# Kernel tuning notes

Measured on AMD Instinct MI355X. Metric: run time of the kernel, lower is better.

The kernel has to match this reference:

```python
import jax, jax.numpy as jnp
import numpy as np

IN_F = 4096
OUT_F = 4096
PACKED_IN = IN_F // 16  # 16 ternary values per int32 (2 bits each)
TOKENS = 8192


def _pack(vals_int32):
    # vals_int32: [out, packed_in, 16] with entries in {0,1,2}
    shifts = (jnp.arange(16, dtype=jnp.int32) * 2)
    return jnp.sum(vals_int32 << shifts, axis=-1).astype(jnp.int32)


def _unpack_weight(packed, scale, in_features):
    # packed: [out, packed_in] int32 -> fp32 weight [out, in_features]
    shifts = (jnp.arange(16, dtype=jnp.int32) * 2)
    vals = (packed[:, :, None] >> shifts) & 3           # [out, packed_in, 16]
    w = vals.reshape(packed.shape[0], -1)[:, :in_features]
    return (w.astype(jnp.float32) - 1.0) * scale


def setup_inputs() -> dict:
    key = jax.random.key(0)
    k1, k2 = jax.random.split(key)
    x = jax.random.normal(k1, (TOKENS, IN_F), dtype=jnp.float32)
    # mapped ternary values in {0,1,2} (i.e. w_ternary + 1), packed 2-bit
    mapped = jax.random.randint(k2, (OUT_F, PACKED_IN, 16), 0, 3, dtype=jnp.int32)
    packed_weight = _pack(mapped)
    scale = jnp.float32(0.02)
    return {"x": x, "packed_weight": packed_weight, "scale": scale}


def reference(x, packed_weight, scale):
    # dequantize ternary weight
    w = _unpack_weight(packed_weight, scale, IN_F)      # [out, in]
    # abs-max activation scaling along the last dim
    x_scale = jnp.clip(jnp.max(jnp.abs(x), axis=-1, keepdims=True), 1e-5, None)
    x_scaled = x / x_scale
    out = jnp.einsum('ti,oi->to', x_scaled, w)          # F.linear (no bias)
    return out * x_scale
```

## Files before the change

kernel.cpp:

```cpp
#include <hip/hip_runtime.h>
#include <math.h>

typedef __attribute__((ext_vector_type(4)))  int   i32x4;
typedef __attribute__((ext_vector_type(16))) int   i32x16;
typedef __attribute__((ext_vector_type(4)))  float f32x4;

namespace {
constexpr int IN_F   = 4096;
constexpr int OUT_F  = 4096;
constexpr int TOKENS = 8192;
constexpr int PACKED = IN_F / 16;

constexpr int BM   = 256;
constexpr int BN   = 128;
constexpr int BK   = 128;
constexpr int NTHR = 256;
constexpr int NT   = IN_F / BK;

constexpr size_t XQ_BYTES = (size_t)TOKENS * IN_F;
constexpr size_t XS_BYTES = (size_t)TOKENS * 4;
constexpr size_t BQ_OFF   = XQ_BYTES + XS_BYTES;
constexpr size_t BQ_BYTES = (size_t)PACKED * OUT_F * 16;
constexpr size_t WS_NEED  = BQ_OFF + BQ_BYTES;
}

__device__ __forceinline__ i32x4 unpack16(unsigned w) {
  i32x4 r;
#pragma unroll
  for (int g = 0; g < 4; ++g) {
    unsigned t = (w >> (8 * g)) & 0xFFu;
    unsigned s = (t | (t << 6) | (t << 12) | (t << 18)) & 0x03030303u;
    r[g] = (int)((((s | 0x80808080u) - 0x01010101u) ^ 0x80808080u));
  }
  return r;
}

__global__ __launch_bounds__(256)
void rowquant(const float* __restrict__ X, signed char* __restrict__ XQ,
              float* __restrict__ XS) {
  __shared__ float smax[4];
  const int row = blockIdx.x;
  const int t   = threadIdx.x;
  const float* xr = X + (size_t)row * IN_F + t * 16;

  f32x4 v[4];
  float m = 0.f;
#pragma unroll
  for (int j = 0; j < 4; ++j) {
    v[j] = *(const f32x4*)(xr + j * 4);
    m = fmaxf(m, fmaxf(fmaxf(fabsf(v[j].x), fabsf(v[j].y)),
                       fmaxf(fabsf(v[j].z), fabsf(v[j].w))));
  }
#pragma unroll
  for (int off = 32; off; off >>= 1) m = fmaxf(m, __shfl_xor(m, off, 64));
  if ((t & 63) == 0) smax[t >> 6] = m;
  __syncthreads();
  m = fmaxf(fmaxf(smax[0], smax[1]), fmaxf(smax[2], smax[3]));
  m = fmaxf(m, 1e-5f);
  const float r = 127.f / m;

  i32x4 d;
#pragma unroll
  for (int j = 0; j < 4; ++j) {
    int q0 = (int)rintf(v[j].x * r);
    int q1 = (int)rintf(v[j].y * r);
    int q2 = (int)rintf(v[j].z * r);
    int q3 = (int)rintf(v[j].w * r);
    d[j] = (q0 & 255) | ((q1 & 255) << 8) | ((q2 & 255) << 16) | ((q3 & 255) << 24);
  }
  *(i32x4*)(XQ + (size_t)row * IN_F + t * 16) = d;
  if (t == 0) XS[row] = m;
}

__global__ __launch_bounds__(256)
void unpackB(const unsigned* __restrict__ PW, signed char* __restrict__ BQ) {
  const int g = blockIdx.x * 256 + threadIdx.x;
  const int c = g >> 12;
  const int n = g & 4095;
  i32x4 u = unpack16(PW[(size_t)n * PACKED + c]);
  *(i32x4*)(BQ + ((size_t)c * OUT_F + n) * 16) = u;
}

#define STAGE_A(BUF, KT)                                                        \
  {                                                                             \
    _Pragma("unroll")                                                           \
    for (int cc = 0; cc < 2; ++cc) {                                            \
      const int c_ = w * 2 + cc;                                                \
      _Pragma("unroll")                                                         \
      for (int rb = 0; rb < 4; ++rb) {                                          \
        const signed char* src =                                                \
            XQ + (size_t)(m0 + rb * 64 + lane) * IN_F + (KT) * BK + c_ * 16;    \
        signed char* dst = lA + (BUF) * 32768 + c_ * 4096 + rb * 1024;          \
        __builtin_amdgcn_global_load_lds(                                       \
            (const __attribute__((address_space(1))) void*)src,                 \
            (__attribute__((address_space(3))) void*)dst, 16, 0, 0);            \
      }                                                                         \
    }                                                                           \
  }

#define LOAD_B(B, KT)                                                           \
  {                                                                             \
    _Pragma("unroll")                                                           \
    for (int nf = 0; nf < 2; ++nf) {                                            \
      _Pragma("unroll")                                                         \
      for (int ks = 0; ks < 4; ++ks)                                            \
        B[nf][ks] = *(const i32x4*)(BQ +                                        \
            ((size_t)((KT) * 8 + ks * 2 + h) * OUT_F + nrow[nf]) * 16);         \
      }                                                                         \
  }

#define COMPUTE_TILE(BUFOFF, B)                                                 \
  {                                                                             \
    _Pragma("unroll")                                                           \
    for (int ks = 0; ks < 4; ++ks) {                                            \
      i32x4 afr[4];                                                             \
      _Pragma("unroll")                                                         \
      for (int mf = 0; mf < 4; ++mf)                                            \
        afr[mf] = *(const i32x4*)(lA + (BUFOFF) + (ks * 2 + h) * 4096 +         \
                                  (wm * 128 + mf * 32 + l31) * 16);             \
      _Pragma("unroll")                                                         \
      for (int mf = 0; mf < 4; ++mf) {                                          \
        acc[mf][0] = __builtin_amdgcn_mfma_i32_32x32x32_i8(afr[mf], B[0][ks],   \
                                                           acc[mf][0], 0, 0, 0);\
        acc[mf][1] = __builtin_amdgcn_mfma_i32_32x32x32_i8(afr[mf], B[1][ks],   \
                                                           acc[mf][1], 0, 0, 0);\
      }                                                                         \
    }                                                                           \
  }

__global__ __launch_bounds__(NTHR, 2)
void gemm_i8(const signed char* __restrict__ XQ, const signed char* __restrict__ BQ,
             const float* __restrict__ XS, const float* __restrict__ SC,
             float* __restrict__ OUT) {
  __shared__ signed char lA[2 * 32768];

  const int tid  = threadIdx.x;
  const int lane = tid & 63;
  const int w    = tid >> 6;
  const int wm   = w >> 1;
  const int wn   = w & 1;
  const int l31  = lane & 31;
  const int h    = lane >> 5;

  const int orig = blockIdx.y * gridDim.x + blockIdx.x;
  const int xcd  = orig & 7;
  const int idx  = orig >> 3;
  const int m0   = (idx >> 2) * BM;
  const int n0   = (xcd * 4 + (idx & 3)) * BN;

  const int nrow[2] = { n0 + wn * 64 + 0 * 32 + l31,
                        n0 + wn * 64 + 1 * 32 + l31 };

  i32x16 acc[4][2];
#pragma unroll
  for (int mf = 0; mf < 4; ++mf)
#pragma unroll
    for (int nf = 0; nf < 2; ++nf)
      acc[mf][nf] = (i32x16)(0);

  i32x4 Ba[2][4], Bb[2][4];

  STAGE_A(0, 0);
  LOAD_B(Ba, 0);

  for (int kt = 0; kt < NT; kt += 2) {
    STAGE_A(1, kt + 1);
    LOAD_B(Bb, kt + 1);
    asm volatile("s_waitcnt vmcnt(16)" ::: "memory");
    __builtin_amdgcn_s_barrier();
    COMPUTE_TILE(0, Ba);
    asm volatile("" ::: "memory");
    __builtin_amdgcn_s_barrier();

    if (kt + 2 < NT) {
      STAGE_A(0, kt + 2);
      LOAD_B(Ba, kt + 2);
      asm volatile("s_waitcnt vmcnt(16)" ::: "memory");
    } else {
      asm volatile("s_waitcnt vmcnt(0)" ::: "memory");
    }
    __builtin_amdgcn_s_barrier();
    COMPUTE_TILE(32768, Bb);
    asm volatile("" ::: "memory");
    __builtin_amdgcn_s_barrier();
  }

  const float sc = SC[0] / 127.f;
#pragma unroll
  for (int mf = 0; mf < 4; ++mf) {
    float fs[16];
#pragma unroll
    for (int r = 0; r < 16; ++r) {
      const int mm = m0 + wm * 128 + mf * 32 + 4 * h + (r & 3) + 8 * (r >> 2);
      fs[r] = sc * XS[mm];
    }
#pragma unroll
    for (int nf = 0; nf < 2; ++nf) {
      const int ncol = n0 + wn * 64 + nf * 32 + l31;
#pragma unroll
      for (int r = 0; r < 16; ++r) {
        const int mm = m0 + wm * 128 + mf * 32 + 4 * h + (r & 3) + 8 * (r >> 2);
        OUT[(size_t)mm * OUT_F + ncol] = (float)acc[mf][nf][r] * fs[r];
      }
    }
  }
}

__global__ __launch_bounds__(NTHR, 2)
void gemm_i8_pw(const signed char* __restrict__ XQ, const unsigned* __restrict__ PW,
                const float* __restrict__ XS, const float* __restrict__ SC,
                float* __restrict__ OUT) {
  __shared__ signed char lA[BM * BK];

  const int tid  = threadIdx.x;
  const int lane = tid & 63;
  const int w    = tid >> 6;
  const int wm   = w >> 1;
  const int wn   = w & 1;
  const int l31  = lane & 31;
  const int h    = lane >> 5;

  const int m0 = blockIdx.y * BM;
  const int n0 = blockIdx.x * BN;

  i32x16 acc[4][2];
#pragma unroll
  for (int mf = 0; mf < 4; ++mf)
#pragma unroll
    for (int nf = 0; nf < 2; ++nf)
      acc[mf][nf] = (i32x16)(0);

  const unsigned* pb0 = PW + (size_t)(n0 + wn * 64 + 0 * 32 + l31) * PACKED;
  const unsigned* pb1 = PW + (size_t)(n0 + wn * 64 + 1 * 32 + l31) * PACKED;

  for (int kt = 0; kt < IN_F / BK; ++kt) {
#pragma unroll
    for (int cc = 0; cc < 2; ++cc) {
      const int c = w * 2 + cc;
#pragma unroll
      for (int rb = 0; rb < 4; ++rb) {
        const signed char* src =
            XQ + (size_t)(m0 + rb * 64 + lane) * IN_F + kt * BK + c * 16;
        signed char* dst = lA + c * 4096 + rb * 1024;
        __builtin_amdgcn_global_load_lds(
            (const __attribute__((address_space(1))) void*)src,
            (__attribute__((address_space(3))) void*)dst, 16, 0, 0);
      }
    }

    unsigned bw0[4], bw1[4];
#pragma unroll
    for (int ks = 0; ks < 4; ++ks) {
      bw0[ks] = pb0[kt * 8 + ks * 2 + h];
      bw1[ks] = pb1[kt * 8 + ks * 2 + h];
    }

    __syncthreads();

#pragma unroll
    for (int ks = 0; ks < 4; ++ks) {
      i32x4 bfr0 = unpack16(bw0[ks]);
      i32x4 bfr1 = unpack16(bw1[ks]);
      i32x4 afr[4];
#pragma unroll
      for (int mf = 0; mf < 4; ++mf)
        afr[mf] = *(const i32x4*)(lA + (ks * 2 + h) * 4096 +
                                  (wm * 128 + mf * 32 + l31) * 16);
#pragma unroll
      for (int mf = 0; mf < 4; ++mf) {
        acc[mf][0] = __builtin_amdgcn_mfma_i32_32x32x32_i8(afr[mf], bfr0, acc[mf][0], 0, 0, 0);
        acc[mf][1] = __builtin_amdgcn_mfma_i32_32x32x32_i8(afr[mf], bfr1, acc[mf][1], 0, 0, 0);
      }
    }
    __syncthreads();
  }

  const float sc = SC[0] / 127.f;
#pragma unroll
  for (int mf = 0; mf < 4; ++mf) {
    float fs[16];
#pragma unroll
    for (int r = 0; r < 16; ++r) {
      const int mm = m0 + wm * 128 + mf * 32 + 4 * h + (r & 3) + 8 * (r >> 2);
      fs[r] = sc * XS[mm];
    }
#pragma unroll
    for (int nf = 0; nf < 2; ++nf) {
      const int ncol = n0 + wn * 64 + nf * 32 + l31;
#pragma unroll
      for (int r = 0; r < 16; ++r) {
        const int mm = m0 + wm * 128 + mf * 32 + 4 * h + (r & 3) + 8 * (r >> 2);
        OUT[(size_t)mm * OUT_F + ncol] = (float)acc[mf][nf][r] * fs[r];
      }
    }
  }
}

extern "C" void kernel_launch(void* const* d_in, const int* in_sizes, int n_in,
                              void* d_out, int out_size, void* d_ws, size_t ws_size,
                              hipStream_t stream) {
  const float*    x  = (const float*)d_in[0];
  const unsigned* pw = (const unsigned*)d_in[1];
  const float*    sc = (const float*)d_in[2];
  float*          out = (float*)d_out;

  signed char* xq = (signed char*)d_ws;
  float*       xs = (float*)((char*)d_ws + XQ_BYTES);

  rowquant<<<dim3(TOKENS), dim3(256), 0, stream>>>(x, xq, xs);

  dim3 grid(OUT_F / BN, TOKENS / BM);
  if (ws_size >= WS_NEED) {
    signed char* bq = (signed char*)d_ws + BQ_OFF;
    unpackB<<<dim3(OUT_F * PACKED / 256), dim3(256), 0, stream>>>(pw, bq);
    gemm_i8<<<grid, dim3(NTHR), 0, stream>>>(xq, bq, xs, sc, out);
  } else {
    gemm_i8_pw<<<grid, dim3(NTHR), 0, stream>>>(xq, pw, xs, sc, out);
  }
}
```

Before: 419.7 us.

## Shrink GEMM tiles to 256x64x64, add MFMA priority, warp-per-row quantize

The int8 GEMM block tile shrinks from 256x128 (BK 128) to 256x64 (BK 64). Each wave now owns a 64x64 slice, LDS use is halved and occupancy is raised to 3 blocks per SIMD, and the XCD swizzle is remapped for the larger grid. s_setprio is placed around the MFMA bursts. The row-quantize kernel now handles one row per wave, which removes the shared-memory reduction and a barrier. Smaller tiles lower arithmetic intensity and increase redundant A/B traffic, in exchange for better latency hiding and tail balance.

```diff
diff --git a/kernel.cpp b/kernel.cpp
--- a/kernel.cpp
+++ b/kernel.cpp
@@ -12,8 +12,8 @@
 constexpr int PACKED = IN_F / 16;
 
 constexpr int BM   = 256;
-constexpr int BN   = 128;
-constexpr int BK   = 128;
+constexpr int BN   = 64;
+constexpr int BK   = 64;
 constexpr int NTHR = 256;
 constexpr int NT   = IN_F / BK;
 
@@ -38,38 +38,33 @@
 __global__ __launch_bounds__(256)
 void rowquant(const float* __restrict__ X, signed char* __restrict__ XQ,
               float* __restrict__ XS) {
-  __shared__ float smax[4];
-  const int row = blockIdx.x;
-  const int t   = threadIdx.x;
-  const float* xr = X + (size_t)row * IN_F + t * 16;
-
-  f32x4 v[4];
+  const int row  = blockIdx.x * 4 + (threadIdx.x >> 6);
+  const int lane = threadIdx.x & 63;
+  const float* xr = X + (size_t)row * IN_F;
+
+  f32x4 v[16];
   float m = 0.f;
 #pragma unroll
-  for (int j = 0; j < 4; ++j) {
-    v[j] = *(const f32x4*)(xr + j * 4);
-    m = fmaxf(m, fmaxf(fmaxf(fabsf(v[j].x), fabsf(v[j].y)),
-                       fmaxf(fabsf(v[j].z), fabsf(v[j].w))));
+  for (int c = 0; c < 16; ++c) {
+    v[c] = *(const f32x4*)(xr + c * 256 + lane * 4);
+    m = fmaxf(m, fmaxf(fmaxf(fabsf(v[c].x), fabsf(v[c].y)),
+                       fmaxf(fabsf(v[c].z), fabsf(v[c].w))));
   }
 #pragma unroll
   for (int off = 32; off; off >>= 1) m = fmaxf(m, __shfl_xor(m, off, 64));
-  if ((t & 63) == 0) smax[t >> 6] = m;
-  __syncthreads();
-  m = fmaxf(fmaxf(smax[0], smax[1]), fmaxf(smax[2], smax[3]));
   m = fmaxf(m, 1e-5f);
   const float r = 127.f / m;
 
-  i32x4 d;
-#pragma unroll
-  for (int j = 0; j < 4; ++j) {
-    int q0 = (int)rintf(v[j].x * r);
-    int q1 = (int)rintf(v[j].y * r);
-    int q2 = (int)rintf(v[j].z * r);
-    int q3 = (int)rintf(v[j].w * r);
-    d[j] = (q0 & 255) | ((q1 & 255) << 8) | ((q2 & 255) << 16) | ((q3 & 255) << 24);
-  }
-  *(i32x4*)(XQ + (size_t)row * IN_F + t * 16) = d;
-  if (t == 0) XS[row] = m;
+#pragma unroll
+  for (int c = 0; c < 16; ++c) {
+    int q0 = (int)rintf(v[c].x * r);
+    int q1 = (int)rintf(v[c].y * r);
+    int q2 = (int)rintf(v[c].z * r);
+    int q3 = (int)rintf(v[c].w * r);
+    unsigned d = (q0 & 255) | ((q1 & 255) << 8) | ((q2 & 255) << 16) | ((q3 & 255) << 24);
+    *(unsigned*)(XQ + (size_t)row * IN_F + c * 256 + lane * 4) = d;
+  }
+  if (lane == 0) XS[row] = m;
 }
 
 __global__ __launch_bounds__(256)
@@ -81,20 +76,17 @@
   *(i32x4*)(BQ + ((size_t)c * OUT_F + n) * 16) = u;
 }
 
+
 #define STAGE_A(BUF, KT)                                                        \
   {                                                                             \
     _Pragma("unroll")                                                           \
-    for (int cc = 0; cc < 2; ++cc) {                                            \
-      const int c_ = w * 2 + cc;                                                \
-      _Pragma("unroll")                                                         \
-      for (int rb = 0; rb < 4; ++rb) {                                          \
-        const signed char* src =                                                \
-            XQ + (size_t)(m0 + rb * 64 + lane) * IN_F + (KT) * BK + c_ * 16;    \
-        signed char* dst = lA + (BUF) * 32768 + c_ * 4096 + rb * 1024;          \
-        __builtin_amdgcn_global_load_lds(                                       \
-            (const __attribute__((address_space(1))) void*)src,                 \
-            (__attribute__((address_space(3))) void*)dst, 16, 0, 0);            \
-      }                                                                         \
+    for (int rb = 0; rb < 4; ++rb) {                                            \
+      const signed char* src =                                                  \
+          XQ + (size_t)(m0 + rb * 64 + lane) * IN_F + (KT) * BK + w * 16;       \
+      signed char* dst = lA + (BUF) * 16384 + w * 4096 + rb * 1024;             \
+      __builtin_amdgcn_global_load_lds(                                         \
+          (const __attribute__((address_space(1))) void*)src,                   \
+          (__attribute__((address_space(3))) void*)dst, 16, 0, 0);              \
     }                                                                           \
   }
 
@@ -103,36 +95,113 @@
     _Pragma("unroll")                                                           \
     for (int nf = 0; nf < 2; ++nf) {                                            \
       _Pragma("unroll")                                                         \
-      for (int ks = 0; ks < 4; ++ks)                                            \
+      for (int ks = 0; ks < 2; ++ks)                                            \
         B[nf][ks] = *(const i32x4*)(BQ +                                        \
-            ((size_t)((KT) * 8 + ks * 2 + h) * OUT_F + nrow[nf]) * 16);         \
+            ((size_t)((KT) * 4 + ks * 2 + h) * OUT_F + nrow[nf]) * 16);         \
       }                                                                         \
   }
 
 #define COMPUTE_TILE(BUFOFF, B)                                                 \
   {                                                                             \
     _Pragma("unroll")                                                           \
-    for (int ks = 0; ks < 4; ++ks) {                                            \
-      i32x4 afr[4];                                                             \
+    for (int ks = 0; ks < 2; ++ks) {                                            \
+      i32x4 afr[2];                                                             \
       _Pragma("unroll")                                                         \
-      for (int mf = 0; mf < 4; ++mf)                                            \
+      for (int mf = 0; mf < 2; ++mf)                                            \
         afr[mf] = *(const i32x4*)(lA + (BUFOFF) + (ks * 2 + h) * 4096 +         \
-                                  (wm * 128 + mf * 32 + l31) * 16);             \
+                                  (w * 64 + mf * 32 + l31) * 16);               \
+      __builtin_amdgcn_s_setprio(1);                                            \
       _Pragma("unroll")                                                         \
-      for (int mf = 0; mf < 4; ++mf) {                                          \
+      for (int mf = 0; mf < 2; ++mf) {                                          \
         acc[mf][0] = __builtin_amdgcn_mfma_i32_32x32x32_i8(afr[mf], B[0][ks],   \
                                                            acc[mf][0], 0, 0, 0);\
         acc[mf][1] = __builtin_amdgcn_mfma_i32_32x32x32_i8(afr[mf], B[1][ks],   \
                                                            acc[mf][1], 0, 0, 0);\
       }                                                                         \
+      __builtin_amdgcn_s_setprio(0);                                            \
     }                                                                           \
   }
 
-__global__ __launch_bounds__(NTHR, 2)
+__global__ __launch_bounds__(NTHR, 3)
 void gemm_i8(const signed char* __restrict__ XQ, const signed char* __restrict__ BQ,
              const float* __restrict__ XS, const float* __restrict__ SC,
              float* __restrict__ OUT) {
-  __shared__ signed char lA[2 * 32768];
+  __shared__ signed char lA[2 * 16384];
+
+  const int tid  = threadIdx.x;
+  const int lane = tid & 63;
+  const int w    = tid >> 6;
+  const int l31  = lane & 31;
+  const int h    = lane >> 5;
+
+  const int orig = blockIdx.y * gridDim.x + blockIdx.x;
+  const int xcd  = orig & 7;
+  const int idx  = orig >> 3;
+  const int m0   = (idx >> 3) * BM;
+  const int n0   = (xcd * 8 + (idx & 7)) * BN;
+
+  const int nrow[2] = { n0 + 0 * 32 + l31, n0 + 1 * 32 + l31 };
+
+  i32x16 acc[2][2];
+#pragma unroll
+  for (int mf = 0; mf < 2; ++mf)
+#pragma unroll
+    for (int nf = 0; nf < 2; ++nf)
+      acc[mf][nf] = (i32x16)(0);
+
+  i32x4 Ba[2][2], Bb[2][2];
+
+  STAGE_A(0, 0);
+  LOAD_B(Ba, 0);
+
+  for (int kt = 0; kt < NT; kt += 2) {
+    STAGE_A(1, kt + 1);
+    LOAD_B(Bb, kt + 1);
+    asm volatile("s_waitcnt vmcnt(8)" ::: "memory");
+    __builtin_amdgcn_s_barrier();
+    COMPUTE_TILE(0, Ba);
+    asm volatile("" ::: "memory");
+    __builtin_amdgcn_s_barrier();
+
+    if (kt + 2 < NT) {
+      STAGE_A(0, kt + 2);
+      LOAD_B(Ba, kt + 2);
+      asm volatile("s_waitcnt vmcnt(8)" ::: "memory");
+    } else {
+      asm volatile("s_waitcnt vmcnt(0)" ::: "memory");
+    }
+    __builtin_amdgcn_s_barrier();
+    COMPUTE_TILE(16384, Bb);
+    asm volatile("" ::: "memory");
+    __builtin_amdgcn_s_barrier();
+  }
+
+  const float sc = SC[0] / 127.f;
+#pragma unroll
+  for (int mf = 0; mf < 2; ++mf) {
+    float fs[16];
+#pragma unroll
+    for (int r = 0; r < 16; ++r) {
+      const int mm = m0 + w * 64 + mf * 32 + 4 * h + (r & 3) + 8 * (r >> 2);
+      fs[r] = sc * XS[mm];
+    }
+#pragma unroll
+    for (int nf = 0; nf < 2; ++nf) {
+      const int ncol = n0 + nf * 32 + l31;
+#pragma unroll
+      for (int r = 0; r < 16; ++r) {
+        const int mm = m0 + w * 64 + mf * 32 + 4 * h + (r & 3) + 8 * (r >> 2);
+        OUT[(size_t)mm * OUT_F + ncol] = (float)acc[mf][nf][r] * fs[r];
+      }
+    }
+  }
+}
+
+__global__ __launch_bounds__(256, 2)
+void gemm_i8_pw(const signed char* __restrict__ XQ, const unsigned* __restrict__ PW,
+                const float* __restrict__ XS, const float* __restrict__ SC,
+                float* __restrict__ OUT) {
+  __shared__ signed char lA[256 * 128];
 
   const int tid  = threadIdx.x;
   const int lane = tid & 63;
@@ -142,14 +211,8 @@
   const int l31  = lane & 31;
   const int h    = lane >> 5;
 
-  const int orig = blockIdx.y * gridDim.x + blockIdx.x;
-  const int xcd  = orig & 7;
-  const int idx  = orig >> 3;
-  const int m0   = (idx >> 2) * BM;
-  const int n0   = (xcd * 4 + (idx & 3)) * BN;
-
-  const int nrow[2] = { n0 + wn * 64 + 0 * 32 + l31,
-                        n0 + wn * 64 + 1 * 32 + l31 };
+  const int m0 = blockIdx.y * 256;
+  const int n0 = blockIdx.x * 128;
 
   i32x16 acc[4][2];
 #pragma unroll
@@ -158,89 +221,17 @@
     for (int nf = 0; nf < 2; ++nf)
       acc[mf][nf] = (i32x16)(0);
 
-  i32x4 Ba[2][4], Bb[2][4];
-
-  STAGE_A(0, 0);
-  LOAD_B(Ba, 0);
-
-  for (int kt = 0; kt < NT; kt += 2) {
-    STAGE_A(1, kt + 1);
-    LOAD_B(Bb, kt + 1);
-    asm volatile("s_waitcnt vmcnt(16)" ::: "memory");
-    __builtin_amdgcn_s_barrier();
-    COMPUTE_TILE(0, Ba);
-    asm volatile("" ::: "memory");
-    __builtin_amdgcn_s_barrier();
-
-    if (kt + 2 < NT) {
-      STAGE_A(0, kt + 2);
-      LOAD_B(Ba, kt + 2);
-      asm volatile("s_waitcnt vmcnt(16)" ::: "memory");
-    } else {
-      asm volatile("s_waitcnt vmcnt(0)" ::: "memory");
-    }
-    __builtin_amdgcn_s_barrier();
-    COMPUTE_TILE(32768, Bb);
-    asm volatile("" ::: "memory");
-    __builtin_amdgcn_s_barrier();
-  }
-
-  const float sc = SC[0] / 127.f;
-#pragma unroll
-  for (int mf = 0; mf < 4; ++mf) {
-    float fs[16];
-#pragma unroll
-    for (int r = 0; r < 16; ++r) {
-      const int mm = m0 + wm * 128 + mf * 32 + 4 * h + (r & 3) + 8 * (r >> 2);
-      fs[r] = sc * XS[mm];
-    }
-#pragma unroll
-    for (int nf = 0; nf < 2; ++nf) {
-      const int ncol = n0 + wn * 64 + nf * 32 + l31;
-#pragma unroll
-      for (int r = 0; r < 16; ++r) {
-        const int mm = m0 + wm * 128 + mf * 32 + 4 * h + (r & 3) + 8 * (r >> 2);
-        OUT[(size_t)mm * OUT_F + ncol] = (float)acc[mf][nf][r] * fs[r];
-      }
-    }
-  }
-}
-
-__global__ __launch_bounds__(NTHR, 2)
-void gemm_i8_pw(const signed char* __restrict__ XQ, const unsigned* __restrict__ PW,
-                const float* __restrict__ XS, const float* __restrict__ SC,
-                float* __restrict__ OUT) {
-  __shared__ signed char lA[BM * BK];
-
-  const int tid  = threadIdx.x;
-  const int lane = tid & 63;
-  const int w    = tid >> 6;
-  const int wm   = w >> 1;
-  const int wn   = w & 1;
-  const int l31  = lane & 31;
-  const int h    = lane >> 5;
-
-  const int m0 = blockIdx.y * BM;
-  const int n0 = blockIdx.x * BN;
-
-  i32x16 acc[4][2];
-#pragma unroll
-  for (int mf = 0; mf < 4; ++mf)
-#pragma unroll
-    for (int nf = 0; nf < 2; ++nf)
-      acc[mf][nf] = (i32x16)(0);
-
   const unsigned* pb0 = PW + (size_t)(n0 + wn * 64 + 0 * 32 + l31) * PACKED;
   const unsigned* pb1 = PW + (size_t)(n0 + wn * 64 + 1 * 32 + l31) * PACKED;
 
-  for (int kt = 0; kt < IN_F / BK; ++kt) {
+  for (int kt = 0; kt < IN_F / 128; ++kt) {
 #pragma unroll
     for (int cc = 0; cc < 2; ++cc) {
       const int c = w * 2 + cc;
 #pragma unroll
       for (int rb = 0; rb < 4; ++rb) {
         const signed char* src =
-            XQ + (size_t)(m0 + rb * 64 + lane) * IN_F + kt * BK + c * 16;
+            XQ + (size_t)(m0 + rb * 64 + lane) * IN_F + kt * 128 + c * 16;
         signed char* dst = lA + c * 4096 + rb * 1024;
         __builtin_amdgcn_global_load_lds(
             (const __attribute__((address_space(1))) void*)src,
@@ -307,14 +298,15 @@
   signed char* xq = (signed char*)d_ws;
   float*       xs = (float*)((char*)d_ws + XQ_BYTES);
 
-  rowquant<<<dim3(TOKENS), dim3(256), 0, stream>>>(x, xq, xs);
-
-  dim3 grid(OUT_F / BN, TOKENS / BM);
+  rowquant<<<dim3(TOKENS / 4), dim3(256), 0, stream>>>(x, xq, xs);
+
   if (ws_size >= WS_NEED) {
     signed char* bq = (signed char*)d_ws + BQ_OFF;
     unpackB<<<dim3(OUT_F * PACKED / 256), dim3(256), 0, stream>>>(pw, bq);
+    dim3 grid(OUT_F / BN, TOKENS / BM);
     gemm_i8<<<grid, dim3(NTHR), 0, stream>>>(xq, bq, xs, sc, out);
   } else {
-    gemm_i8_pw<<<grid, dim3(NTHR), 0, stream>>>(xq, pw, xs, sc, out);
-  }
-}
+    dim3 grid(OUT_F / 128, TOKENS / 256);
+    gemm_i8_pw<<<grid, dim3(256), 0, stream>>>(xq, pw, xs, sc, out);
+  }
+}
```

After: 538.4 us. +28.3%, slower.
